# Optimization experiments

Hardware: AMD Instinct MI355X
Metric: run time of the kernel (lower is better)

Reference implementation:

```python
import jax, jax.numpy as jnp
import numpy as np

IMG = 64        # img_size
D_STEPS = 64    # cnfg['d_steps']
D_MAX = 1.0     # cnfg['d_max']


def _consts():
    f = 70.0 * (IMG / 64.0)
    c = IMG / 2.0 - 0.5
    K = jnp.array([[f, 0.0, c], [0.0, f, c], [0.0, 0.0, 1.0]], jnp.float32)
    K_inv = jnp.linalg.inv(K)
    R_t = jnp.eye(3, dtype=jnp.float32)          # transpose(cnfg['R']) with R=I
    t = jnp.array([[0.0], [0.0], [2.5]], jnp.float32)  # cnfg['t'][:,None]
    return K, K_inv, R_t, t


def _rot_mat(alphas):
    # get_rotation_mat: Z-axis rotation by pi*alpha, (BS,3,3)
    a = jnp.pi * alphas
    c, s = jnp.cos(a), jnp.sin(a)
    z, o = jnp.zeros_like(a), jnp.ones_like(a)
    return jnp.stack([
        jnp.stack([c, -s, z], -1),
        jnp.stack([s, c, z], -1),
        jnp.stack([z, z, o], -1)], -2)


def _pred_depth_from_samplegrid(sdfvalues, Z_coords):
    # sdfvalues: (BS,H,W,D,1), Z_coords: (BS,H,W,D)
    pnts_out = jnp.where(sdfvalues > 0.0, 1.0, -1.0)
    # sign change + -> - along depth axis (zero crossing entering the surface)
    zc = (pnts_out[..., :-1, :] - pnts_out[..., 1:, :] == 2.0).astype(sdfvalues.dtype)
    occ = jnp.max(zc, axis=-2)                       # (BS,H,W,1)
    Zc = Z_coords[..., None]                         # (BS,H,W,D,1)
    zeros = jnp.zeros_like(zc[..., 0:1, :])

    def helper(zcross):
        tmp = 100.0 * (1.0 - zcross)
        depth = jnp.min(Zc * zcross + tmp, axis=-2)
        sdf = jnp.sum(sdfvalues * zcross, axis=-2)
        return sdf, depth

    s1, d1 = helper(jnp.concatenate([zc, zeros], axis=-2))
    s2, d2 = helper(jnp.concatenate([zeros, zc], axis=-2))
    eps = 1e-06
    depth_pred = occ * (d1 - s1 / (s2 - s1 - eps) * (d2 - d1))
    return depth_pred, occ


def _render(z_shape, z_extr, W1, b1, W2, b2):
    K, K_inv, R_t, t = _consts()
    BS = z_shape.shape[0]
    # get_obj_trans
    s_obj = (1.0 / z_extr[:, 0]).reshape(BS, 1, 1, 1)
    t_obj = z_extr[:, 1:4].reshape(BS, 1, 3, 1)
    R_obj = _rot_mat(z_extr[:, 4])                   # (BS,3,3)
    s_inv = 1.0 / s_obj
    R_obj_inv = jnp.linalg.inv(R_obj)
    # bounding-box depth offset (mean camera-space depth of 9 bbox points)
    corners = jnp.array([[1., 1., 1.], [1., 1., -1.], [1., -1., 1.], [1., -1., -1.],
                         [-1., 1., 1.], [-1., 1., -1.], [-1., -1., 1.], [-1., -1., -1.],
                         [0., 0., 0.]], jnp.float32)
    Xbb = jnp.broadcast_to(corners[None, :, :, None], (BS, 9, 3, 1))
    Xbb = jnp.einsum('bij,bajk->baik', R_obj_inv, s_inv * Xbb) + t_obj
    Xbb = jnp.einsum('ij,bajk->baik', jnp.linalg.inv(R_t), Xbb) + t
    Xbb = jnp.einsum('ij,bajk->baik', K, Xbb)
    bb_depth = jnp.mean(Xbb[:, :, 2:3], axis=1, keepdims=True)  # (BS,1,1,1)
    # image coordinate grid (full image; bbox crop has data-dependent shape)
    xs = jnp.linspace(0.0, IMG - 1.0, IMG)
    zs = jnp.linspace(-D_MAX, D_MAX, D_STEPS)
    Xg, Yg, Zg = jnp.meshgrid(xs, xs, zs)            # 'xy' indexing, (IMG,IMG,D)
    n = IMG * IMG
    coords_2d = jnp.stack([Xg.reshape(-1), Yg.reshape(-1)], -1)  # (n*D,2)
    coords_2d = jnp.broadcast_to(coords_2d[None], (BS, n * D_STEPS, 2))
    Z = Zg.reshape(1, n, D_STEPS, 1) * s_inv + bb_depth          # (BS,n,D,1)
    depth = Z.reshape(BS, n * D_STEPS, 1)
    coords_3d = jnp.concatenate([coords_2d, jnp.ones_like(depth)], axis=-1)
    # trans_pnts: pixel+depth -> world -> object coords
    X = coords_3d[..., None]                                     # (BS,N,3,1)
    X = jnp.einsum('ij,bajk->baik', K_inv, X)
    X = jnp.einsum('ij,bajk->baik', R_t, depth[..., None] * X - t)
    X = s_obj * jnp.einsum('bij,bajk->baik', R_obj, X - t_obj)
    X = X[..., 0]                                                # (BS,N,3)
    # deepsdf stub MLP on concat([X, z_shape])
    zt = jnp.broadcast_to(z_shape[:, None, :], (BS, X.shape[1], z_shape.shape[-1]))
    feat = jnp.concatenate([X, zt], axis=-1)                     # (BS,N,64)
    h = jax.nn.relu(jnp.einsum('bnf,fh->bnh', feat, W1) + b1)
    sdf = jnp.tanh(jnp.einsum('bnh,ho->bno', h, W2) + b2)        # (BS,N,1)
    sdf = sdf.reshape(BS, IMG, IMG, D_STEPS, 1)
    Zc = Z.reshape(BS, IMG, IMG, D_STEPS)
    depth_pred, occ = _pred_depth_from_samplegrid(sdf, Zc)
    return depth_pred, occ


def setup_inputs() -> dict:
    key = jax.random.key(0)
    k1, k2, k3, k4 = jax.random.split(key, 4)
    BS, D_SH, H1 = 4, 61, 128
    z_shape = jax.random.normal(k1, (BS, D_SH), jnp.float32)
    u = jax.random.uniform(k2, (BS, 5), jnp.float32)
    # scale in [0.75,1.25), translations in [-0.25,0.25), alpha in [0,1)
    z_extr = jnp.concatenate([0.75 + 0.5 * u[:, 0:1],
                              0.5 * (u[:, 1:4] - 0.5),
                              u[:, 4:5]], axis=1)
    W1 = 0.3 * jax.random.normal(k3, (3 + D_SH, H1), jnp.float32)
    b1 = jnp.zeros((H1,), jnp.float32)
    W2 = 0.3 * jax.random.normal(k4, (H1, 1), jnp.float32)
    b2 = jnp.zeros((1,), jnp.float32)
    return {"z_shape": z_shape, "z_extr": z_extr, "W1": W1, "b1": b1, "W2": W2, "b2": b2}


def reference(z_shape, z_extr, W1, b1, W2, b2):
    return _render(z_shape, z_extr, W1, b1, W2, b2)
```

## Files before the change

kernel.cpp:

```cpp
#include <hip/hip_runtime.h>
#include <math.h>


#define N_RAYS (4 * 64 * 64)

typedef float v2f __attribute__((ext_vector_type(2)));
typedef float f4v __attribute__((ext_vector_type(4)));

static __device__ __forceinline__ v2f mk2(float a, float b) {
    v2f r; r.x = a; r.y = b; return r;
}

#define SLOAD4(dst, ptr) \
    asm volatile("s_load_dwordx4 %0, %1, 0x0" : "=s"(dst) : "s"(ptr))

__global__ __launch_bounds__(512) void precompute_cvec(
    const float* __restrict__ z_shape,
    const float* __restrict__ W1,
    const float* __restrict__ b1,
    float* __restrict__ cvec)
{
    int tid = blockIdx.x * blockDim.x + threadIdx.x;
    if (tid >= 4 * 128) return;
    int b = tid >> 7;
    int h = tid & 127;
    float acc = b1[h];
    #pragma unroll
    for (int f = 0; f < 61; ++f)
        acc = fmaf(z_shape[b * 61 + f], W1[(3 + f) * 128 + h], acc);
    cvec[tid] = acc;
}

__global__ __launch_bounds__(256, 8) void render_kernel(
    const float* __restrict__ z_extr,
    const float* __restrict__ W1,
    const float* __restrict__ W2,
    const float* __restrict__ b2,
    const float* __restrict__ cvec,
    float* __restrict__ out)
{
    const int tid  = threadIdx.x;
    const int lane = tid & 63;
    const int wave = __builtin_amdgcn_readfirstlane(tid >> 6);
    const int ray  = blockIdx.x * 4 + wave;
    const int b    = ray >> 12;
    const int rem  = ray & 4095;
    const int yi   = rem >> 6;
    const int xj   = rem & 63;

    const float scale = z_extr[b * 5 + 0];
    const float tx    = z_extr[b * 5 + 1];
    const float ty    = z_extr[b * 5 + 2];
    const float tz    = z_extr[b * 5 + 3];
    const float alpha = z_extr[b * 5 + 4];

    const float a  = 3.14159274101257324f * alpha;
    const float ca = cosf(a);
    const float sa = sinf(a);
    const float s_obj = 1.0f / scale;
    const float s_inv = 1.0f / s_obj;
    const float T = tz + 2.5f;

    const float step = 2.0f / 63.0f;
    const float zk  = -1.0f + (float)lane * step;
    const float Z   = zk * s_inv + T;
    const float zk1 = -1.0f + (float)(lane + 1) * step;
    const float Z1  = zk1 * s_inv + T;

    const float kf  = 1.0f / 70.0f;
    const float kc  = -(31.5f / 70.0f);
    const float u = fmaf((float)xj, kf, kc);
    const float v = fmaf((float)yi, kf, kc);

    const float qx = Z * u - tx;
    const float qy = Z * v - ty;
    const float qz = (Z - 2.5f) - tz;
    const float X0 = s_obj * (ca * qx - sa * qy);
    const float X1 = s_obj * (sa * qx + ca * qy);
    const float X2 = s_obj * qz;

    const v2f X0v = mk2(X0, X0);
    const v2f X1v = mk2(X1, X1);
    const v2f X2v = mk2(X2, X2);
    const v2f zero2 = mk2(0.0f, 0.0f);

    const float* __restrict__ cb = cvec + b * 128;

    float acc = b2[0];
    #pragma unroll 4
    for (int q = 0; q < 16; ++q) {
        const int o = q * 8;
        f4v a0l, a0h, a1l, a1h, a2l, a2h, ccl, cch, wol, woh;
        SLOAD4(a0l, W1 + o);            SLOAD4(a0h, W1 + o + 4);
        SLOAD4(a1l, W1 + 128 + o);      SLOAD4(a1h, W1 + 128 + o + 4);
        SLOAD4(a2l, W1 + 256 + o);      SLOAD4(a2h, W1 + 256 + o + 4);
        SLOAD4(ccl, cb + o);            SLOAD4(cch, cb + o + 4);
        SLOAD4(wol, W2 + o);            SLOAD4(woh, W2 + o + 4);
        asm volatile("s_waitcnt lgkmcnt(0)"
                     : "+s"(a0l), "+s"(a0h), "+s"(a1l), "+s"(a1h),
                       "+s"(a2l), "+s"(a2h), "+s"(ccl), "+s"(cch),
                       "+s"(wol), "+s"(woh));

        {
            v2f lo = __builtin_elementwise_fma(X2v, mk2(a2l.x, a2l.y), mk2(ccl.x, ccl.y));
            lo = __builtin_elementwise_fma(X1v, mk2(a1l.x, a1l.y), lo);
            lo = __builtin_elementwise_fma(X0v, mk2(a0l.x, a0l.y), lo);
            lo = __builtin_elementwise_max(lo, zero2);
            v2f hi = __builtin_elementwise_fma(X2v, mk2(a2l.z, a2l.w), mk2(ccl.z, ccl.w));
            hi = __builtin_elementwise_fma(X1v, mk2(a1l.z, a1l.w), hi);
            hi = __builtin_elementwise_fma(X0v, mk2(a0l.z, a0l.w), hi);
            hi = __builtin_elementwise_max(hi, zero2);
            acc = fmaf(lo.x, wol.x, acc);
            acc = fmaf(lo.y, wol.y, acc);
            acc = fmaf(hi.x, wol.z, acc);
            acc = fmaf(hi.y, wol.w, acc);
        }
        {
            v2f lo = __builtin_elementwise_fma(X2v, mk2(a2h.x, a2h.y), mk2(cch.x, cch.y));
            lo = __builtin_elementwise_fma(X1v, mk2(a1h.x, a1h.y), lo);
            lo = __builtin_elementwise_fma(X0v, mk2(a0h.x, a0h.y), lo);
            lo = __builtin_elementwise_max(lo, zero2);
            v2f hi = __builtin_elementwise_fma(X2v, mk2(a2h.z, a2h.w), mk2(cch.z, cch.w));
            hi = __builtin_elementwise_fma(X1v, mk2(a1h.z, a1h.w), hi);
            hi = __builtin_elementwise_fma(X0v, mk2(a0h.z, a0h.w), hi);
            hi = __builtin_elementwise_max(hi, zero2);
            acc = fmaf(lo.x, woh.x, acc);
            acc = fmaf(lo.y, woh.y, acc);
            acc = fmaf(hi.x, woh.z, acc);
            acc = fmaf(hi.y, woh.w, acc);
        }
    }
    const float sdf = tanhf(acc);

    const unsigned long long mask  = __ballot(sdf > 0.0f);
    const unsigned long long cross = mask & ~(mask >> 1) & 0x7fffffffffffffffULL;

    const bool isC = (cross >> lane) & 1ULL;
    const float sdf_next = __shfl_down(sdf, 1, 64);

    float d1 = isC ? Z        : 100.0f;
    float d2 = isC ? Z1       : 100.0f;
    float s1 = isC ? sdf      : 0.0f;
    float s2 = isC ? sdf_next : 0.0f;

    #pragma unroll
    for (int m = 1; m < 64; m <<= 1) {
        d1 = fminf(d1, __shfl_xor(d1, m, 64));
        d2 = fminf(d2, __shfl_xor(d2, m, 64));
        s1 += __shfl_xor(s1, m, 64);
        s2 += __shfl_xor(s2, m, 64);
    }

    if (lane == 0) {
        float occ = (cross != 0ULL) ? 1.0f : 0.0f;
        float depth = 0.0f;
        if (cross != 0ULL)
            depth = d1 - s1 / (s2 - s1 - 1e-6f) * (d2 - d1);
        out[ray]          = depth;
        out[N_RAYS + ray] = occ;
    }
}

extern "C" void kernel_launch(void* const* d_in, const int* in_sizes, int n_in,
                              void* d_out, int out_size, void* d_ws, size_t ws_size,
                              hipStream_t stream) {
    const float* z_shape = (const float*)d_in[0];
    const float* z_extr  = (const float*)d_in[1];
    const float* W1      = (const float*)d_in[2];
    const float* b1      = (const float*)d_in[3];
    const float* W2      = (const float*)d_in[4];
    const float* b2      = (const float*)d_in[5];
    float* out  = (float*)d_out;
    float* cvec = (float*)d_ws;

    precompute_cvec<<<1, 512, 0, stream>>>(z_shape, W1, b1, cvec);
    render_kernel<<<N_RAYS / 4, 256, 0, stream>>>(z_extr, W1, W2, b2, cvec, out);
}
```

Before: 87.43 us.

## Fuse latent projection into render kernel via LDS and early-exit empty rays

Removes the separate single-block precompute kernel and has each block recompute the 128-entry shape-latent projection into LDS, then read it from LDS instead of through scalar loads. This saves a launch and the dependency between the two kernels, but every one of the 4096 blocks now repeats a 61-step matvec per hidden unit, which adds redundant global reads and ALU work before a barrier. It also takes the sign test on the pre-tanh accumulator and exits early for rays with no surface crossing, skipping the tanh and the shuffle reductions. The LDS reads of cvec are per-lane vector loads of uniform data, which may be slower than the former scalar loads.

Result: no change. 88.47 us (+1.2%).

```diff
diff --git a/kernel.cpp b/kernel.cpp
--- a/kernel.cpp
+++ b/kernel.cpp
@@ -14,31 +14,17 @@
 #define SLOAD4(dst, ptr) \
     asm volatile("s_load_dwordx4 %0, %1, 0x0" : "=s"(dst) : "s"(ptr))
 
-__global__ __launch_bounds__(512) void precompute_cvec(
+__global__ __launch_bounds__(256, 8) void render_fused(
     const float* __restrict__ z_shape,
+    const float* __restrict__ z_extr,
     const float* __restrict__ W1,
     const float* __restrict__ b1,
-    float* __restrict__ cvec)
-{
-    int tid = blockIdx.x * blockDim.x + threadIdx.x;
-    if (tid >= 4 * 128) return;
-    int b = tid >> 7;
-    int h = tid & 127;
-    float acc = b1[h];
-    #pragma unroll
-    for (int f = 0; f < 61; ++f)
-        acc = fmaf(z_shape[b * 61 + f], W1[(3 + f) * 128 + h], acc);
-    cvec[tid] = acc;
-}
-
-__global__ __launch_bounds__(256, 8) void render_kernel(
-    const float* __restrict__ z_extr,
-    const float* __restrict__ W1,
     const float* __restrict__ W2,
     const float* __restrict__ b2,
-    const float* __restrict__ cvec,
     float* __restrict__ out)
 {
+    __shared__ __align__(16) float cvec_lds[128];
+
     const int tid  = threadIdx.x;
     const int lane = tid & 63;
     const int wave = __builtin_amdgcn_readfirstlane(tid >> 6);
@@ -47,6 +33,17 @@
     const int rem  = ray & 4095;
     const int yi   = rem >> 6;
     const int xj   = rem & 63;
+
+    if (tid < 128) {
+        const int h  = tid;
+        const int bb = blockIdx.x >> 10;
+        const float* __restrict__ zs = z_shape + bb * 61;
+        float a = b1[h];
+        #pragma unroll 4
+        for (int f = 0; f < 61; ++f)
+            a = fmaf(zs[f], W1[(3 + f) * 128 + h], a);
+        cvec_lds[h] = a;
+    }
 
     const float scale = z_extr[b * 5 + 0];
     const float tx    = z_extr[b * 5 + 1];
@@ -84,22 +81,22 @@
     const v2f X2v = mk2(X2, X2);
     const v2f zero2 = mk2(0.0f, 0.0f);
 
-    const float* __restrict__ cb = cvec + b * 128;
+    __syncthreads();
 
     float acc = b2[0];
     #pragma unroll 4
     for (int q = 0; q < 16; ++q) {
         const int o = q * 8;
-        f4v a0l, a0h, a1l, a1h, a2l, a2h, ccl, cch, wol, woh;
+        f4v a0l, a0h, a1l, a1h, a2l, a2h, wol, woh;
         SLOAD4(a0l, W1 + o);            SLOAD4(a0h, W1 + o + 4);
         SLOAD4(a1l, W1 + 128 + o);      SLOAD4(a1h, W1 + 128 + o + 4);
         SLOAD4(a2l, W1 + 256 + o);      SLOAD4(a2h, W1 + 256 + o + 4);
-        SLOAD4(ccl, cb + o);            SLOAD4(cch, cb + o + 4);
         SLOAD4(wol, W2 + o);            SLOAD4(woh, W2 + o + 4);
+        const f4v ccl = *(const f4v*)(cvec_lds + o);
+        const f4v cch = *(const f4v*)(cvec_lds + o + 4);
         asm volatile("s_waitcnt lgkmcnt(0)"
                      : "+s"(a0l), "+s"(a0h), "+s"(a1l), "+s"(a1h),
-                       "+s"(a2l), "+s"(a2h), "+s"(ccl), "+s"(cch),
-                       "+s"(wol), "+s"(woh));
+                       "+s"(a2l), "+s"(a2h), "+s"(wol), "+s"(woh));
 
         {
             v2f lo = __builtin_elementwise_fma(X2v, mk2(a2l.x, a2l.y), mk2(ccl.x, ccl.y));
@@ -130,11 +127,19 @@
             acc = fmaf(hi.y, woh.w, acc);
         }
     }
-    const float sdf = tanhf(acc);
 
-    const unsigned long long mask  = __ballot(sdf > 0.0f);
+    const unsigned long long mask  = __ballot(acc > 0.0f);
     const unsigned long long cross = mask & ~(mask >> 1) & 0x7fffffffffffffffULL;
 
+    if (cross == 0ULL) {
+        if (lane == 0) {
+            out[ray]          = 0.0f;
+            out[N_RAYS + ray] = 0.0f;
+        }
+        return;
+    }
+
+    const float sdf = tanhf(acc);
     const bool isC = (cross >> lane) & 1ULL;
     const float sdf_next = __shfl_down(sdf, 1, 64);
 
@@ -152,12 +157,8 @@
     }
 
     if (lane == 0) {
-        float occ = (cross != 0ULL) ? 1.0f : 0.0f;
-        float depth = 0.0f;
-        if (cross != 0ULL)
-            depth = d1 - s1 / (s2 - s1 - 1e-6f) * (d2 - d1);
-        out[ray]          = depth;
-        out[N_RAYS + ray] = occ;
+        out[ray]          = d1 - s1 / (s2 - s1 - 1e-6f) * (d2 - d1);
+        out[N_RAYS + ray] = 1.0f;
     }
 }
 
@@ -171,8 +172,7 @@
     const float* W2      = (const float*)d_in[4];
     const float* b2      = (const float*)d_in[5];
     float* out  = (float*)d_out;
-    float* cvec = (float*)d_ws;
+    (void)d_ws; (void)ws_size;
 
-    precompute_cvec<<<1, 512, 0, stream>>>(z_shape, W1, b1, cvec);
-    render_kernel<<<N_RAYS / 4, 256, 0, stream>>>(z_extr, W1, W2, b2, cvec, out);
+    render_fused<<<N_RAYS / 4, 256, 0, stream>>>(z_shape, z_extr, W1, b1, W2, b2, out);
 }
```
